# Optimization experiments

Hardware: AMD Instinct MI355X
Metric: run time of the kernel (lower is better)

## Reference

```python
import jax, jax.numpy as jnp
from jax import lax
import numpy as np

B, HW = 256, 64          # batch, image side (grayscale)
L, E, K = 32, 64, 8192   # latent_size, embedding_size, num_embeddings
DN = ('NHWC', 'HWIO', 'NHWC')


def setup_inputs() -> dict:
    key = jax.random.key(0)
    ks = jax.random.split(key, 21)
    n = lambda k, shape, s=0.05: (jax.random.normal(k, shape, jnp.float32) * s)
    return {
        'x': jax.random.uniform(ks[0], (B, HW, HW), jnp.float32),
        # encoder convs (SAME, stride 2): 64->32->16->8
        'enc_w1': n(ks[1], (4, 4, 1, 32)),   'enc_b1': jnp.zeros((32,), jnp.float32),
        'enc_w2': n(ks[2], (4, 4, 32, 64)),  'enc_b2': jnp.zeros((64,), jnp.float32),
        'enc_w3': n(ks[3], (4, 4, 64, 128)), 'enc_b3': jnp.zeros((128,), jnp.float32),
        # encoder dense: flatten 8*8*128=8192 -> 512 -> L*E=2048
        'fc_w': n(ks[4], (8192, 512), 0.02), 'fc_b': jnp.zeros((512,), jnp.float32),
        'ffc_w': n(ks[5], (512, L * E), 0.02), 'ffc_b': jnp.zeros((L * E,), jnp.float32),
        # VQ codebook
        'embeds': n(ks[6], (K, E), 0.02),
        # decoder dense: 2048 -> 512, then 1x1x512 feature map
        'dec_fc_w': n(ks[7], (L * E, 512), 0.02), 'dec_fc_b': jnp.zeros((512,), jnp.float32),
        # decoder conv_transpose VALID: 1->4->16->64
        'dec_w1': n(ks[8], (4, 4, 512, 256)),  'dec_b1': jnp.zeros((256,), jnp.float32),
        'dec_w2': n(ks[9], (4, 4, 256, 128)),  'dec_b2': jnp.zeros((128,), jnp.float32),
        'dec_w3': n(ks[10], (4, 4, 128, 1)),   'dec_b3': jnp.zeros((1,), jnp.float32),
    }


def _conv(h, w, b, s):
    return jax.nn.relu(lax.conv_general_dilated(h, w, (s, s), 'SAME', dimension_numbers=DN) + b)


def reference(x, enc_w1, enc_b1, enc_w2, enc_b2, enc_w3, enc_b3,
              fc_w, fc_b, ffc_w, ffc_b, embeds,
              dec_fc_w, dec_fc_b, dec_w1, dec_b1, dec_w2, dec_b2, dec_w3, dec_b3):
    # ---- encoder ----
    h = x[..., None]                                   # (B,64,64,1)
    h = _conv(h, enc_w1, enc_b1, 2)                    # (B,32,32,32)
    h = _conv(h, enc_w2, enc_b2, 2)                    # (B,16,16,64)
    h = _conv(h, enc_w3, enc_b3, 2)                    # (B,8,8,128)
    h = h.reshape(h.shape[0], -1)                      # (B,8192)
    h = jax.nn.relu(h @ fc_w + fc_b)                   # (B,512)
    pred = jax.nn.relu(h @ ffc_w + ffc_b).reshape(-1, L, E)  # (B,L,E)
    # ---- VQ middle: nearest codebook entry (argmin of L2 norm == argmin of squared dist) ----
    d2 = (jnp.sum(pred * pred, axis=-1, keepdims=True)
          - 2.0 * jnp.einsum('ble,ke->blk', pred, embeds)
          + jnp.sum(embeds * embeds, axis=-1))         # (B,L,K)
    classes = jnp.argmin(d2, axis=-1)                  # (B,L) int
    collected = embeds[classes]                        # (B,L,E) gather
    h = collected.reshape(-1, L * E)                   # (B,2048)
    # ---- decoder ----
    h = jax.nn.relu(h @ dec_fc_w + dec_fc_b)           # (B,512)
    h = h[:, None, None, :]                            # (B,1,1,512)
    h = jax.nn.relu(lax.conv_transpose(h, dec_w1, (1, 1), 'VALID', dimension_numbers=DN) + dec_b1)  # (B,4,4,256)
    h = jax.nn.relu(lax.conv_transpose(h, dec_w2, (4, 4), 'VALID', dimension_numbers=DN) + dec_b2)  # (B,16,16,128)
    out = lax.conv_transpose(h, dec_w3, (4, 4), 'VALID', dimension_numbers=DN) + dec_b3             # (B,64,64,1)
    return out  # L2 loss_type: output_t = logits_t
```

## Files before the change

kernel.cpp:

```cpp
#include <hip/hip_runtime.h>
#include <cfloat>


typedef short bf16x8 __attribute__((ext_vector_type(8)));
typedef float f32x4 __attribute__((ext_vector_type(4)));
#define MFMA16(a, b, c) __builtin_amdgcn_mfma_f32_16x16x32_bf16(a, b, c, 0, 0, 0)

__device__ inline unsigned short f2bf(float x) {
  unsigned u = __float_as_uint(x);
  u += 0x7fffu + ((u >> 16) & 1u);
  return (unsigned short)(u >> 16);
}
__device__ inline float bf2f(unsigned short h) {
  return __uint_as_float(((unsigned)h) << 16);
}
__device__ inline void split3v(float v, unsigned short& hb, unsigned short& mb,
                               unsigned short& lb) {
  hb = f2bf(v);
  float r1 = v - bf2f(hb);
  mb = f2bf(r1);
  lb = f2bf(r1 - bf2f(mb));
}

#define PB0 12672
#define PB1 (PB0 + 13056)
#define PB2 (PB1 + 128)
#define PB3 (PB2 + 512)
#define PB4 (PB3 + 2048)
#define PB5 (PB4 + 32)
#define PB6 (PB5 + 4096)
#define PB7 (PB6 + 2048)
__global__ __launch_bounds__(256) void k_prep_early(
    const float* __restrict__ enc_w2, const float* __restrict__ enc_w3,
    const float* __restrict__ embeds, const float* __restrict__ dec_fc_w,
    const float* __restrict__ dec_w2, unsigned short* __restrict__ h1base,
    unsigned short* __restrict__ h2base, unsigned short* __restrict__ Wp2H,
    unsigned short* __restrict__ Wp2M, unsigned short* __restrict__ Wp2L,
    unsigned short* __restrict__ Wp3H, unsigned short* __restrict__ Wp3M,
    unsigned short* __restrict__ Wp3L, unsigned short* __restrict__ eB,
    float* __restrict__ n2, unsigned short* __restrict__ Bp_dfc,
    unsigned short* __restrict__ Bp_d2) {
  int blk = blockIdx.x;
  int t = threadIdx.x;
  if (blk < PB0) {
    int li = blk * 256 + t;
    int bc = li & 8191;
    int rest = li >> 13;
    int i = rest % 132, plane = rest / 132;
    int b = bc >> 5, c = bc & 31;
    int row, col;
    if (i < 34) { row = 0; col = i; }
    else if (i < 68) { row = 33; col = i - 34; }
    else { int j = i - 68; row = 1 + (j >> 1); col = (j & 1) ? 33 : 0; }
    h1base[(size_t)plane * 9469952 + ((size_t)(b * 34 + row) * 34 + col) * 32 + c] = 0;
  } else if (blk < PB1) {
    int li = (blk - PB0) * 256 + t;
    int bc = li & 16383;
    int rest = li >> 14;
    int i = rest % 68, plane = rest / 68;
    int b = bc >> 6, c = bc & 63;
    int row, col;
    if (i < 18) { row = 0; col = i; }
    else if (i < 36) { row = 17; col = i - 18; }
    else { int j = i - 36; row = 1 + (j >> 1); col = (j & 1) ? 17 : 0; }
    h2base[(size_t)plane * 5308416 + ((size_t)(b * 18 + row) * 18 + col) * 64 + c] = 0;
  } else if (blk < PB2) {
    int idx = (blk - PB1) * 256 + t;
    int j = idx & 7, lane = (idx >> 3) & 63, nt = (idx >> 9) & 3, s = idx >> 11;
    int ci = ((lane >> 4) << 3) + j, co = (nt << 4) + (lane & 15);
    unsigned short hb, mb, lb;
    split3v(enc_w2[(s * 32 + ci) * 64 + co], hb, mb, lb);
    Wp2H[idx] = hb; Wp2M[idx] = mb; Wp2L[idx] = lb;
  } else if (blk < PB3) {
    int idx = (blk - PB2) * 256 + t;
    int j = idx & 7, lane = (idx >> 3) & 63, ks = (idx >> 9) & 1;
    int nt = (idx >> 10) & 3, ch = (idx >> 12) & 1, s = idx >> 13;
    int ci = ks * 32 + ((lane >> 4) << 3) + j;
    int co = ch * 64 + (nt << 4) + (lane & 15);
    unsigned short hb, mb, lb;
    split3v(enc_w3[(s * 64 + ci) * 128 + co], hb, mb, lb);
    Wp3H[idx] = hb; Wp3M[idx] = mb; Wp3L[idx] = lb;
  } else if (blk < PB4) {
    int idx = (blk - PB3) * 256 + t;
    int j = idx & 7, lane = (idx >> 3) & 63;
    int f = idx >> 9;
    int nt = f & 3, ks = (f >> 2) & 1, kt = f >> 3;
    int code = kt * 64 + nt * 16 + (lane & 15);
    int k = ks * 32 + ((lane >> 4) << 3) + j;
    unsigned short hb, mb, lb;
    split3v(embeds[(size_t)code * 64 + k], hb, mb, lb);
    size_t base = (size_t)f * 1536 + lane * 8 + j;
    eB[base] = hb; eB[base + 512] = mb; eB[base + 1024] = lb;
  } else if (blk < PB5) {
    int k = (blk - PB4) * 256 + t;
    const float4* p = (const float4*)(embeds + (size_t)k * 64);
    float s0 = 0, s1 = 0, s2 = 0, s3 = 0;
#pragma unroll
    for (int j = 0; j < 16; ++j) {
      float4 v = p[j];
      s0 = fmaf(v.x, v.x, s0); s1 = fmaf(v.y, v.y, s1);
      s2 = fmaf(v.z, v.z, s2); s3 = fmaf(v.w, v.w, s3);
    }
    n2[k] = (s0 + s1) + (s2 + s3);
  } else if (blk < PB6) {
    int idx = (blk - PB5) * 256 + t;
    int j = idx & 7, lane = (idx >> 3) & 63;
    int f = idx >> 9;
    int ntg = f & 31;
    int kt = f >> 5;
    int k = kt * 32 + ((lane >> 4) << 3) + j;
    int n = ntg * 16 + (lane & 15);
    unsigned short hb, mb, lb;
    split3v(dec_fc_w[(size_t)k * 512 + n], hb, mb, lb);
    Bp_dfc[idx] = hb; Bp_dfc[idx + 1048576] = mb;
  } else if (blk < PB7) {
    int idx = (blk - PB6) * 256 + t;
    int j = idx & 7, lane = (idx >> 3) & 63;
    int f = idx >> 9;
    int ntg = f & 127;
    int kt = f >> 7;
    int k = kt * 32 + ((lane >> 4) << 3) + j;
    int n = ntg * 16 + (lane & 15);
    int o = n & 127, ru = n >> 7;
    int r = ru >> 2, u = ru & 3;
    int sf = (3 - r) * 4 + (3 - u);
    unsigned short hb, mb, lb;
    split3v(dec_w2[(((size_t)sf * 256 + k) << 7) + o], hb, mb, lb);
    Bp_d2[idx] = hb; Bp_d2[idx + 524288] = mb;
  }
}

__global__ __launch_bounds__(256) void k_conv1(const float* __restrict__ x,
                                               const float* __restrict__ w,
                                               const float* __restrict__ bias,
                                               unsigned short* __restrict__ oH,
                                               unsigned short* __restrict__ oM,
                                               unsigned short* __restrict__ oL) {
  int b = blockIdx.x >> 5;
  int y = blockIdx.x & 31;
  int t = threadIdx.x;
  int c = t & 31;
  int xg = t >> 5;
  float acc[4] = {0.f, 0.f, 0.f, 0.f};
  for (int dy = 0; dy < 4; ++dy) {
    int iy = 2 * y + dy - 1;
    if (iy < 0 || iy >= 64) continue;
    const float* xrow = x + ((size_t)b * 64 + iy) * 64;
    for (int dx = 0; dx < 4; ++dx) {
      float wv = w[(dy * 4 + dx) * 32 + c];
#pragma unroll
      for (int i = 0; i < 4; ++i) {
        int ix = 8 * xg + 2 * i + dx - 1;
        float v = (ix >= 0 && ix < 64) ? xrow[ix] : 0.f;
        acc[i] = fmaf(v, wv, acc[i]);
      }
    }
  }
  float bv = bias[c];
#pragma unroll
  for (int i = 0; i < 4; ++i) {
    float v = acc[i] + bv;
    v = v > 0.f ? v : 0.f;
    unsigned short hb, mb, lb;
    split3v(v, hb, mb, lb);
    size_t o = ((size_t)(b * 34 + y + 1) * 34 + (4 * xg + i + 1)) * 32 + c;
    oH[o] = hb; oM[o] = mb; oL[o] = lb;
  }
}

__global__ __launch_bounds__(1024, 4) void k_conv2s(
    const unsigned short* __restrict__ aH, const unsigned short* __restrict__ aM,
    const unsigned short* __restrict__ aL, const unsigned short* __restrict__ wH,
    const unsigned short* __restrict__ wM, const unsigned short* __restrict__ wL,
    const float* __restrict__ bias, unsigned short* __restrict__ oH,
    unsigned short* __restrict__ oM, unsigned short* __restrict__ oL) {
  __shared__ unsigned short Bs[49152];
  int t = threadIdx.x;
  int wave = t >> 6, lane = t & 63;
  int l15 = lane & 15, quad = lane >> 4;
  int m0 = blockIdx.x * 256 + wave * 16;
  int p = m0 + l15;
  int b = p >> 8, y = (p >> 4) & 15, x = p & 15;
  f32x4 acc[4] = {};
#pragma unroll
  for (int hf = 0; hf < 2; ++hf) {
    if (hf) __syncthreads();
    {
      const unsigned short* s0 = wH + hf * 16384;
      const unsigned short* s1 = wM + hf * 16384;
      const unsigned short* s2 = wL + hf * 16384;
#pragma unroll
      for (int i = 0; i < 2; ++i) {
        int o8 = (i * 1024 + t) * 8;
        *(bf16x8*)(Bs + o8)         = *(const bf16x8*)(s0 + o8);
        *(bf16x8*)(Bs + 16384 + o8) = *(const bf16x8*)(s1 + o8);
        *(bf16x8*)(Bs + 32768 + o8) = *(const bf16x8*)(s2 + o8);
      }
    }
    __syncthreads();
#pragma unroll 4
    for (int sl = 0; sl < 8; ++sl) {
      int s = hf * 8 + sl;
      int dy = s >> 2, dx = s & 3;
      size_t aoff = ((size_t)(b * 34 + 2 * y + dy) * 34 + (2 * x + dx)) * 32 + quad * 8;
      bf16x8 ah = *(const bf16x8*)(aH + aoff);
      bf16x8 am = *(const bf16x8*)(aM + aoff);
      bf16x8 al = *(const bf16x8*)(aL + aoff);
#pragma unroll
      for (int nt = 0; nt < 4; ++nt) {
        const unsigned short* bp = Bs + ((sl * 4 + nt) * 64 + lane) * 8;
        bf16x8 bh = *(const bf16x8*)(bp);
        bf16x8 bm = *(const bf16x8*)(bp + 16384);
        bf16x8 bl = *(const bf16x8*)(bp + 32768);
        acc[nt] = MFMA16(am, bm, acc[nt]);
        acc[nt] = MFMA16(ah, bl, acc[nt]);
        acc[nt] = MFMA16(al, bh, acc[nt]);
        acc[nt] = MFMA16(ah, bm, acc[nt]);
        acc[nt] = MFMA16(am, bh, acc[nt]);
        acc[nt] = MFMA16(ah, bh, acc[nt]);
      }
    }
  }
#pragma unroll
  for (int r = 0; r < 4; ++r) {
    int pp = m0 + quad * 4 + r;
    int b2 = pp >> 8, yo = (pp >> 4) & 15, xo = pp & 15;
    size_t obase = ((size_t)(b2 * 18 + yo + 1) * 18 + (xo + 1)) * 64;
#pragma unroll
    for (int nt = 0; nt < 4; ++nt) {
      int co = nt * 16 + l15;
      float v = acc[nt][r] + bias[co];
      v = v > 0.f ? v : 0.f;
      unsigned short hb, mb, lb;
      split3v(v, hb, mb, lb);
      oH[obase + co] = hb; oM[obase + co] = mb; oL[obase + co] = lb;
    }
  }
}

__global__ __launch_bounds__(512, 2) void k_conv3s(
    const unsigned short* __restrict__ aH, const unsigned short* __restrict__ aM,
    const unsigned short* __restrict__ aL, const unsigned short* __restrict__ wH,
    const unsigned short* __restrict__ wM, const unsigned short* __restrict__ wL,
    float* __restrict__ part) {
  __shared__ unsigned short Bs[2][24576];
  int t = threadIdx.x;
  int wave = t >> 6, lane = t & 63;
  int l15 = lane & 15, quad = lane >> 4;
  int ch = wave & 1, mg = wave >> 1;
  int m0 = blockIdx.x * 128 + mg * 32;
  int z = blockIdx.y;
  f32x4 acc[2][4] = {};
  {
    const unsigned short* srcH = wH + (size_t)(z * 8) * 8192;
    const unsigned short* srcM = wM + (size_t)(z * 8) * 8192;
    const unsigned short* srcL = wL + (size_t)(z * 8) * 8192;
#pragma unroll
    for (int i = 0; i < 2; ++i) {
      int o8 = (i * 512 + t) * 8;
      *(bf16x8*)(&Bs[0][o8])         = *(const bf16x8*)(srcH + o8);
      *(bf16x8*)(&Bs[0][8192 + o8])  = *(const bf16x8*)(srcM + o8);
      *(bf16x8*)(&Bs[0][16384 + o8]) = *(const bf16x8*)(srcL + o8);
    }
  }
  __syncthreads();
#pragma unroll 2
  for (int si = 0; si < 8; ++si) {
    int s = z * 8 + si;
    int cur = si & 1, nxt = cur ^ 1;
    bf16x8 stg[6];
    if (si < 7) {
      const unsigned short* srcH = wH + (size_t)(s + 1) * 8192;
      const unsigned short* srcM = wM + (size_t)(s + 1) * 8192;
      const unsigned short* srcL = wL + (size_t)(s + 1) * 8192;
#pragma unroll
      for (int i = 0; i < 2; ++i) {
        int o8 = (i * 512 + t) * 8;
        stg[i]     = *(const bf16x8*)(srcH + o8);
        stg[2 + i] = *(const bf16x8*)(srcM + o8);
        stg[4 + i] = *(const bf16x8*)(srcL + o8);
      }
    }
    int dy = s >> 2, dx = s & 3;
    bf16x8 ah[2][2], am[2][2], al[2][2];
#pragma unroll
    for (int mt = 0; mt < 2; ++mt) {
      int p = m0 + mt * 16 + l15;
      int b = p >> 6, y = (p >> 3) & 7, x = p & 7;
      size_t base = ((size_t)(b * 18 + 2 * y + dy) * 18 + (2 * x + dx)) * 64 + quad * 8;
#pragma unroll
      for (int ks = 0; ks < 2; ++ks) {
        ah[mt][ks] = *(const bf16x8*)(aH + base + ks * 32);
        am[mt][ks] = *(const bf16x8*)(aM + base + ks * 32);
        al[mt][ks] = *(const bf16x8*)(aL + base + ks * 32);
      }
    }
#pragma unroll
    for (int nt = 0; nt < 4; ++nt)
#pragma unroll
      for (int ks = 0; ks < 2; ++ks) {
        const unsigned short* bp =
            &Bs[cur][((ch * 4 + nt) * 2 + ks) * 512 + lane * 8];
        bf16x8 bh = *(const bf16x8*)(bp);
        bf16x8 bm = *(const bf16x8*)(bp + 8192);
        bf16x8 bl = *(const bf16x8*)(bp + 16384);
#pragma unroll
        for (int mt = 0; mt < 2; ++mt) {
          acc[mt][nt] = MFMA16(am[mt][ks], bm, acc[mt][nt]);
          acc[mt][nt] = MFMA16(ah[mt][ks], bl, acc[mt][nt]);
          acc[mt][nt] = MFMA16(al[mt][ks], bh, acc[mt][nt]);
          acc[mt][nt] = MFMA16(ah[mt][ks], bm, acc[mt][nt]);
          acc[mt][nt] = MFMA16(am[mt][ks], bh, acc[mt][nt]);
          acc[mt][nt] = MFMA16(ah[mt][ks], bh, acc[mt][nt]);
        }
      }
    if (si < 7) {
#pragma unroll
      for (int i = 0; i < 2; ++i) {
        int o8 = (i * 512 + t) * 8;
        *(bf16x8*)(&Bs[nxt][o8])         = stg[i];
        *(bf16x8*)(&Bs[nxt][8192 + o8])  = stg[2 + i];
        *(bf16x8*)(&Bs[nxt][16384 + o8]) = stg[4 + i];
      }
    }
    __syncthreads();
  }
  float* Cp = part + (size_t)z * 2097152;
#pragma unroll
  for (int mt = 0; mt < 2; ++mt)
#pragma unroll
    for (int nt = 0; nt < 4; ++nt) {
      int co = ch * 64 + nt * 16 + l15;
#pragma unroll
      for (int r = 0; r < 4; ++r) {
        int pp = m0 + mt * 16 + quad * 4 + r;
        Cp[(size_t)pp * 128 + co] = acc[mt][nt][r];
      }
    }
}

#define FB0 8192
#define FB1 (FB0 + 16384)
__global__ __launch_bounds__(256) void k_prep_fc(
    const float* __restrict__ part, const float* __restrict__ enc_b3,
    unsigned short* __restrict__ h3H, unsigned short* __restrict__ h3M,
    unsigned short* __restrict__ h3L, const float* __restrict__ fc_w,
    unsigned short* __restrict__ Bp_fc) {
  int blk = blockIdx.x;
  int t = threadIdx.x;
  if (blk < FB0) {
    int idx = blk * 256 + t;
    float s = part[idx] + part[2097152 + idx] + enc_b3[idx & 127];
    s = s > 0.f ? s : 0.f;
    unsigned short hb, mb, lb;
    split3v(s, hb, mb, lb);
    h3H[idx] = hb; h3M[idx] = mb; h3L[idx] = lb;
  } else {
    int idx = (blk - FB0) * 256 + t;
    int j = idx & 7, lane = (idx >> 3) & 63;
    int f = idx >> 9;
    int ntg = f & 31;
    int kt = f >> 5;
    int k = kt * 32 + ((lane >> 4) << 3) + j;
    int n = ntg * 16 + (lane & 15);
    unsigned short hb, mb, lb;
    split3v(fc_w[(size_t)k * 512 + n], hb, mb, lb);
    Bp_fc[idx] = hb; Bp_fc[idx + 4194304] = mb; Bp_fc[idx + 8388608] = lb;
  }
}

#define WB0 4096
#define WB1 (WB0 + 8192)
__global__ __launch_bounds__(256) void k_prep_w2(
    const float* __restrict__ ffc_w, unsigned short* __restrict__ Bp_ffc,
    const float* __restrict__ dec_w1, unsigned short* __restrict__ Bp_d1) {
  int blk = blockIdx.x;
  int t = threadIdx.x;
  if (blk < WB0) {
    int idx = blk * 256 + t;
    int j = idx & 7, lane = (idx >> 3) & 63;
    int f = idx >> 9;
    int ntg = f & 127;
    int kt = f >> 7;
    int k = kt * 32 + ((lane >> 4) << 3) + j;
    int n = ntg * 16 + (lane & 15);
    unsigned short hb, mb, lb;
    split3v(ffc_w[(size_t)k * 2048 + n], hb, mb, lb);
    Bp_ffc[idx] = hb; Bp_ffc[idx + 1048576] = mb; Bp_ffc[idx + 2097152] = lb;
  } else {
    int idx = (blk - WB0) * 256 + t;
    int j = idx & 7, lane = (idx >> 3) & 63;
    int f = idx >> 9;
    int ntg = f & 255;
    int kt = f >> 8;
    int k = kt * 32 + ((lane >> 4) << 3) + j;
    int n = ntg * 16 + (lane & 15);
    int o = n & 255, ru = n >> 8;
    int r = ru >> 2, u = ru & 3;
    int sf = (3 - r) * 4 + (3 - u);
    unsigned short hb, mb, lb;
    split3v(dec_w1[(((size_t)sf * 512 + k) << 8) + o], hb, mb, lb);
    Bp_d1[idx] = hb; Bp_d1[idx + 2097152] = mb;
  }
}

template <int NP, int NTW>
__global__ __launch_bounds__(256) void k_mgemm(
    const unsigned short* __restrict__ A0, const unsigned short* __restrict__ A1,
    const unsigned short* __restrict__ A2, const unsigned short* __restrict__ Bp,
    float* __restrict__ C, const float* __restrict__ bias,
    int M, int N, int K, int bmask) {
  int S = gridDim.z;
  int Kc = K / S;
  int t = threadIdx.x;
  int wave = t >> 6, lane = t & 63;
  int l15 = lane & 15, quad = lane >> 4;
  int m0 = blockIdx.x * 64 + wave * 16;
  int n0 = blockIdx.y * (16 * NTW);
  int KT = K >> 5, NT = N >> 4;
  int kt0 = (blockIdx.z * Kc) >> 5;
  int ktn = Kc >> 5;
  size_t sstride = (size_t)KT * NT * 512;
  const unsigned short* arow0 = A0 + (size_t)(m0 + l15) * K + quad * 8;
  const unsigned short* arow1 = A1 + (size_t)(m0 + l15) * K + quad * 8;
  const unsigned short* arow2 = nullptr;
  if constexpr (NP == 3) arow2 = A2 + (size_t)(m0 + l15) * K + quad * 8;
  f32x4 acc[NTW] = {};
  for (int kt = kt0; kt < kt0 + ktn; ++kt) {
    bf16x8 ah = *(const bf16x8*)(arow0 + kt * 32);
    bf16x8 am = *(const bf16x8*)(arow1 + kt * 32);
    bf16x8 al;
    if constexpr (NP == 3) al = *(const bf16x8*)(arow2 + kt * 32);
    const unsigned short* bbase =
        Bp + ((size_t)kt * NT + (n0 >> 4)) * 512 + lane * 8;
#pragma unroll
    for (int nt = 0; nt < NTW; ++nt) {
      const unsigned short* bp = bbase + nt * 512;
      bf16x8 bh = *(const bf16x8*)(bp);
      bf16x8 bm = *(const bf16x8*)(bp + sstride);
      if constexpr (NP == 3) {
        bf16x8 bl = *(const bf16x8*)(bp + 2 * sstride);
        acc[nt] = MFMA16(am, bm, acc[nt]);
        acc[nt] = MFMA16(ah, bl, acc[nt]);
        acc[nt] = MFMA16(al, bh, acc[nt]);
        acc[nt] = MFMA16(ah, bm, acc[nt]);
        acc[nt] = MFMA16(am, bh, acc[nt]);
        acc[nt] = MFMA16(ah, bh, acc[nt]);
      } else {
        acc[nt] = MFMA16(ah, bm, acc[nt]);
        acc[nt] = MFMA16(am, bh, acc[nt]);
        acc[nt] = MFMA16(ah, bh, acc[nt]);
      }
    }
  }
  if (S == 1) {
#pragma unroll
    for (int nt = 0; nt < NTW; ++nt) {
      int n = n0 + nt * 16 + l15;
      float bv = bias[n & bmask];
#pragma unroll
      for (int r = 0; r < 4; ++r) {
        int m = m0 + quad * 4 + r;
        float v = acc[nt][r] + bv;
        C[(size_t)m * N + n] = v > 0.f ? v : 0.f;
      }
    }
  } else {
    float* Cp = C + (size_t)blockIdx.z * M * N;
#pragma unroll
    for (int nt = 0; nt < NTW; ++nt) {
      int n = n0 + nt * 16 + l15;
#pragma unroll
      for (int r = 0; r < 4; ++r) {
        int m = m0 + quad * 4 + r;
        Cp[(size_t)m * N + n] = acc[nt][r];
      }
    }
  }
}

template <int NPOUT>
__global__ __launch_bounds__(256) void k_sumrelu3(
    const float* __restrict__ part, const float* __restrict__ bias,
    unsigned short* __restrict__ oH, unsigned short* __restrict__ oM,
    unsigned short* __restrict__ oL, int MN, int bmask, int S) {
  int idx = blockIdx.x * 256 + threadIdx.x;
  float s = 0.f;
  for (int z = 0; z < S; ++z) s += part[(size_t)z * MN + idx];
  s += bias[idx & bmask];
  s = s > 0.f ? s : 0.f;
  unsigned short hb = f2bf(s);
  float r1 = s - bf2f(hb);
  unsigned short mb = f2bf(r1);
  oH[idx] = hb; oM[idx] = mb;
  if constexpr (NPOUT == 3) oL[idx] = f2bf(r1 - bf2f(mb));
}

__global__ __launch_bounds__(256) void k_vqmfma3(
    const unsigned short* __restrict__ pH, const unsigned short* __restrict__ pM,
    const unsigned short* __restrict__ pL, const unsigned short* __restrict__ eB,
    const float* __restrict__ n2, float* __restrict__ pbd, int* __restrict__ pbk) {
  int t = threadIdx.x;
  int wave = t >> 6, lane = t & 63;
  int l15 = lane & 15, quad = lane >> 4;
  int m0 = blockIdx.x * 128 + wave * 32;
  int z = blockIdx.y;
  bf16x8 ah[2][2], am[2][2], al[2][2];
#pragma unroll
  for (int mt = 0; mt < 2; ++mt) {
    size_t arow = (size_t)(m0 + mt * 16 + l15) * 64 + quad * 8;
#pragma unroll
    for (int ks = 0; ks < 2; ++ks) {
      ah[mt][ks] = *(const bf16x8*)(pH + arow + ks * 32);
      am[mt][ks] = *(const bf16x8*)(pM + arow + ks * 32);
      al[mt][ks] = *(const bf16x8*)(pL + arow + ks * 32);
    }
  }
  float bd[2][4]; int bk[2][4];
#pragma unroll
  for (int mt = 0; mt < 2; ++mt)
#pragma unroll
    for (int r = 0; r < 4; ++r) { bd[mt][r] = FLT_MAX; bk[mt][r] = 0; }
  for (int kt = z * 16; kt < z * 16 + 16; ++kt) {
    const unsigned short* bb = eB + (size_t)kt * 12288 + lane * 8;
    f32x4 acc[2][4] = {};
#pragma unroll
    for (int ks = 0; ks < 2; ++ks)
#pragma unroll
      for (int nt = 0; nt < 4; ++nt) {
        const unsigned short* bp = bb + ((ks * 4 + nt) * 3) * 512;
        bf16x8 bh = *(const bf16x8*)(bp);
        bf16x8 bm = *(const bf16x8*)(bp + 512);
        bf16x8 bl = *(const bf16x8*)(bp + 1024);
#pragma unroll
        for (int mt = 0; mt < 2; ++mt) {
          acc[mt][nt] = MFMA16(am[mt][ks], bm, acc[mt][nt]);
          acc[mt][nt] = MFMA16(ah[mt][ks], bl, acc[mt][nt]);
          acc[mt][nt] = MFMA16(al[mt][ks], bh, acc[mt][nt]);
          acc[mt][nt] = MFMA16(ah[mt][ks], bm, acc[mt][nt]);
          acc[mt][nt] = MFMA16(am[mt][ks], bh, acc[mt][nt]);
          acc[mt][nt] = MFMA16(ah[mt][ks], bh, acc[mt][nt]);
        }
      }
    int cb = kt * 64;
#pragma unroll
    for (int nt = 0; nt < 4; ++nt) {
      int code = cb + nt * 16 + l15;
      float nv = n2[code];
#pragma unroll
      for (int mt = 0; mt < 2; ++mt)
#pragma unroll
        for (int r = 0; r < 4; ++r) {
          float d = fmaf(-2.f, acc[mt][nt][r], nv);
          if (d < bd[mt][r]) { bd[mt][r] = d; bk[mt][r] = code; }
        }
    }
  }
#pragma unroll
  for (int mt = 0; mt < 2; ++mt)
#pragma unroll
    for (int r = 0; r < 4; ++r)
#pragma unroll
      for (int s = 1; s < 16; s <<= 1) {
        float od = __shfl_xor(bd[mt][r], s);
        int ok = __shfl_xor(bk[mt][r], s);
        if (od < bd[mt][r] || (od == bd[mt][r] && ok < bk[mt][r])) {
          bd[mt][r] = od; bk[mt][r] = ok;
        }
      }
  if (l15 == 0) {
#pragma unroll
    for (int mt = 0; mt < 2; ++mt)
#pragma unroll
      for (int r = 0; r < 4; ++r) {
        pbd[(size_t)z * 8192 + m0 + mt * 16 + quad * 4 + r] = bd[mt][r];
        pbk[(size_t)z * 8192 + m0 + mt * 16 + quad * 4 + r] = bk[mt][r];
      }
  }
}

__global__ __launch_bounds__(256) void k_vqgather(const float* __restrict__ pbd,
                                                  const int* __restrict__ pbk,
                                                  const float* __restrict__ embeds,
                                                  unsigned short* __restrict__ cH,
                                                  unsigned short* __restrict__ cM) {
  int idx = blockIdx.x * 256 + threadIdx.x;
  int m = idx >> 6;
  float bd = pbd[m]; int bk = pbk[m];
#pragma unroll
  for (int z = 1; z < 8; ++z) {
    float d = pbd[(size_t)z * 8192 + m]; int k = pbk[(size_t)z * 8192 + m];
    if (d < bd || (d == bd && k < bk)) { bd = d; bk = k; }
  }
  float v = embeds[(size_t)bk * 64 + (idx & 63)];
  unsigned short hb = f2bf(v);
  cH[idx] = hb;
  cM[idx] = f2bf(v - bf2f(hb));
}

__global__ __launch_bounds__(256) void k_dec3(const float* __restrict__ d2buf,
                                              const float* __restrict__ w3,
                                              const float* __restrict__ b3,
                                              float* __restrict__ out) {
  __shared__ float sx[16 * 129];
  __shared__ float wT[128 * 16];
  int b = blockIdx.x >> 4;
  int y = blockIdx.x & 15;
  int t = threadIdx.x;
#pragma unroll
  for (int j = 0; j < 8; ++j) {
    int idx = t + j * 256;
    int xx = idx >> 7, c = idx & 127;
    size_t m2 = ((size_t)b * 4 + (y >> 2)) * 4 + (xx >> 2);
    sx[xx * 129 + c] = d2buf[m2 * 2048 + ((y & 3) * 4 + (xx & 3)) * 128 + c];
  }
#pragma unroll
  for (int j = 0; j < 8; ++j) {
    int idx = t + j * 256;
    int c = idx >> 4, ru = idx & 15;
    int R = ru >> 2, U = ru & 3;
    wT[c * 16 + ru] = w3[((3 - R) * 4 + (3 - U)) * 128 + c];
  }
  __syncthreads();
  int xx = t >> 4, ru = t & 15;
  float a0 = 0, a1 = 0, a2 = 0, a3 = 0;
#pragma unroll 8
  for (int c = 0; c < 128; c += 4) {
    a0 = fmaf(sx[xx * 129 + c + 0], wT[(c + 0) * 16 + ru], a0);
    a1 = fmaf(sx[xx * 129 + c + 1], wT[(c + 1) * 16 + ru], a1);
    a2 = fmaf(sx[xx * 129 + c + 2], wT[(c + 2) * 16 + ru], a2);
    a3 = fmaf(sx[xx * 129 + c + 3], wT[(c + 3) * 16 + ru], a3);
  }
  float acc = (a0 + a1) + (a2 + a3) + b3[0];
  int R = ru >> 2, U = ru & 3;
  out[((size_t)b * 64 + 4 * y + R) * 64 + 4 * xx + U] = acc;
}

extern "C" void kernel_launch(void* const* d_in, const int* in_sizes, int n_in,
                              void* d_out, int out_size, void* d_ws, size_t ws_size,
                              hipStream_t stream) {
  const float* x        = (const float*)d_in[0];
  const float* enc_w1   = (const float*)d_in[1];
  const float* enc_b1   = (const float*)d_in[2];
  const float* enc_w2   = (const float*)d_in[3];
  const float* enc_b2   = (const float*)d_in[4];
  const float* enc_w3   = (const float*)d_in[5];
  const float* enc_b3   = (const float*)d_in[6];
  const float* fc_w     = (const float*)d_in[7];
  const float* fc_b     = (const float*)d_in[8];
  const float* ffc_w    = (const float*)d_in[9];
  const float* ffc_b    = (const float*)d_in[10];
  const float* embeds   = (const float*)d_in[11];
  const float* dec_fc_w = (const float*)d_in[12];
  const float* dec_fc_b = (const float*)d_in[13];
  const float* dec_w1   = (const float*)d_in[14];
  const float* dec_b1   = (const float*)d_in[15];
  const float* dec_w2   = (const float*)d_in[16];
  const float* dec_b2   = (const float*)d_in[17];
  const float* dec_w3   = (const float*)d_in[18];
  const float* dec_b3   = (const float*)d_in[19];
  float* outp = (float*)d_out;

  char* ws = (char*)d_ws;
  size_t off = 0;
  auto alloc = [&](size_t bytes) { size_t r = off; off = (off + bytes + 255) & ~(size_t)255; return r; };

  size_t RA = alloc(57147392);
  unsigned short* h1pH = (unsigned short*)(ws + RA);
  unsigned short* h1pM = (unsigned short*)(ws + RA + 18939904);
  unsigned short* h1pL = (unsigned short*)(ws + RA + 37879808);
  float* d2buf            = (float*)(ws + RA);
  float* partials         = (float*)(ws + RA + 33554432);
  unsigned short* Bp_d1   = (unsigned short*)(ws + RA + 41943040);
  unsigned short* d1H     = (unsigned short*)(ws + RA + 50331648);
  unsigned short* d1M     = (unsigned short*)(ws + RA + 52428800);
  unsigned short* hdH     = (unsigned short*)(ws + RA + 54525952);
  unsigned short* hdM     = (unsigned short*)(ws + RA + 54788096);
  unsigned short* cH      = (unsigned short*)(ws + RA + 55050240);
  unsigned short* cM      = (unsigned short*)(ws + RA + 56098816);

  size_t RB = alloc(31850496);
  unsigned short* h2pH = (unsigned short*)(ws + RB);
  unsigned short* h2pM = (unsigned short*)(ws + RB + 10616832);
  unsigned short* h2pL = (unsigned short*)(ws + RB + 21233664);
  unsigned short* Bp_fc = (unsigned short*)(ws + RB);
  unsigned short* pH    = (unsigned short*)(ws + RB + 28311552);
  unsigned short* pM    = (unsigned short*)(ws + RB + 29360128);
  unsigned short* pL    = (unsigned short*)(ws + RB + 30408704);

  size_t RC = alloc(12582912);
  unsigned short* h3H = (unsigned short*)(ws + RC);
  unsigned short* h3M = (unsigned short*)(ws + RC + 4194304);
  unsigned short* h3L = (unsigned short*)(ws + RC + 8388608);
  unsigned short* Bp_ffc = (unsigned short*)(ws + RC);
  unsigned short* hfcH   = (unsigned short*)(ws + RC + 6291456);
  unsigned short* hfcM   = (unsigned short*)(ws + RC + 6553600);
  unsigned short* hfcL   = (unsigned short*)(ws + RC + 6815744);

  unsigned short* eB     = (unsigned short*)(ws + alloc(3145728));
  unsigned short* Bp_dfc = (unsigned short*)(ws + alloc(4194304));
  unsigned short* Bp_d2  = (unsigned short*)(ws + alloc(2097152));
  float* n2buf   = (float*)(ws + alloc(32768));
  float* pbd     = (float*)(ws + alloc(262144));
  int*   pbk     = (int*)  (ws + alloc(262144));
  unsigned short* Wp2H = (unsigned short*)(ws + alloc(196608));
  unsigned short* Wp2M = Wp2H + 32768;
  unsigned short* Wp2L = Wp2M + 32768;
  unsigned short* Wp3H = (unsigned short*)(ws + alloc(786432));
  unsigned short* Wp3M = Wp3H + 131072;
  unsigned short* Wp3L = Wp3M + 131072;
  (void)ws_size; (void)in_sizes; (void)n_in; (void)out_size;

  k_prep_early<<<PB7, 256, 0, stream>>>(
      enc_w2, enc_w3, embeds, dec_fc_w, dec_w2, h1pH, h2pH,
      Wp2H, Wp2M, Wp2L, Wp3H, Wp3M, Wp3L, eB, n2buf, Bp_dfc, Bp_d2);

  k_conv1<<<8192, 256, 0, stream>>>(x, enc_w1, enc_b1, h1pH, h1pM, h1pL);
  k_conv2s<<<256, 1024, 0, stream>>>(h1pH, h1pM, h1pL, Wp2H, Wp2M, Wp2L,
                                     enc_b2, h2pH, h2pM, h2pL);
  k_conv3s<<<dim3(128, 2), 512, 0, stream>>>(h2pH, h2pM, h2pL,
                                             Wp3H, Wp3M, Wp3L, partials);
  k_prep_fc<<<FB1, 256, 0, stream>>>(partials, enc_b3, h3H, h3M, h3L,
                                     fc_w, Bp_fc);

  k_mgemm<3, 4><<<dim3(4, 8, 16), 256, 0, stream>>>(
      h3H, h3M, h3L, Bp_fc, partials, fc_b, 256, 512, 8192, 511);
  k_prep_w2<<<WB1, 256, 0, stream>>>(ffc_w, Bp_ffc, dec_w1, Bp_d1);
  k_sumrelu3<3><<<512, 256, 0, stream>>>(partials, fc_b, hfcH, hfcM, hfcL,
                                         131072, 511, 16);
  k_mgemm<3, 4><<<dim3(4, 32, 4), 256, 0, stream>>>(
      hfcH, hfcM, hfcL, Bp_ffc, partials, ffc_b, 256, 2048, 512, 2047);
  k_sumrelu3<3><<<2048, 256, 0, stream>>>(partials, ffc_b, pH, pM, pL,
                                          524288, 2047, 4);

  k_vqmfma3<<<dim3(64, 8), 256, 0, stream>>>(pH, pM, pL, eB, n2buf, pbd, pbk);
  k_vqgather<<<2048, 256, 0, stream>>>(pbd, pbk, embeds, cH, cM);

  k_mgemm<2, 4><<<dim3(4, 8, 16), 256, 0, stream>>>(
      cH, cM, nullptr, Bp_dfc, partials, dec_fc_b, 256, 512, 2048, 511);
  k_sumrelu3<2><<<512, 256, 0, stream>>>(partials, dec_fc_b, hdH, hdM, nullptr,
                                         131072, 511, 16);

  k_mgemm<2, 4><<<dim3(4, 64, 2), 256, 0, stream>>>(
      hdH, hdM, nullptr, Bp_d1, partials, dec_b1, 256, 4096, 512, 255);
  k_sumrelu3<2><<<4096, 256, 0, stream>>>(partials, dec_b1, d1H, d1M, nullptr,
                                          1048576, 255, 2);

  k_mgemm<2, 8><<<dim3(64, 16, 1), 256, 0, stream>>>(
      d1H, d1M, nullptr, Bp_d2, d2buf, dec_b2, 4096, 2048, 256, 127);

  k_dec3<<<4096, 256, 0, stream>>>(d2buf, dec_w3, dec_b3, outp);
}
```

Baseline: 431.8 us.

## Stage VQ codebook tiles through double-buffered LDS with register prefetch

The VQ distance kernel used to read codebook fragments straight from global memory in every wave. It now loads each 64-code tile cooperatively into a double-buffered shared-memory array, prefetching the next tile into registers while the MFMAs run on the current one. The launch bounds also request two blocks per SM. This cuts redundant global loads across the four waves and hides load latency, but it adds 48KB of LDS per block, a barrier every iteration, and extra register pressure that may limit occupancy.

```diff
diff --git a/kernel.cpp b/kernel.cpp
--- a/kernel.cpp
+++ b/kernel.cpp
@@ -496,10 +496,11 @@
   if constexpr (NPOUT == 3) oL[idx] = f2bf(r1 - bf2f(mb));
 }
 
-__global__ __launch_bounds__(256) void k_vqmfma3(
+__global__ __launch_bounds__(256, 2) void k_vqmfma3(
     const unsigned short* __restrict__ pH, const unsigned short* __restrict__ pM,
     const unsigned short* __restrict__ pL, const unsigned short* __restrict__ eB,
     const float* __restrict__ n2, float* __restrict__ pbd, int* __restrict__ pbk) {
+  __shared__ unsigned short Es[2][12288];
   int t = threadIdx.x;
   int wave = t >> 6, lane = t & 63;
   int l15 = lane & 15, quad = lane >> 4;
@@ -521,8 +522,28 @@
   for (int mt = 0; mt < 2; ++mt)
 #pragma unroll
     for (int r = 0; r < 4; ++r) { bd[mt][r] = FLT_MAX; bk[mt][r] = 0; }
-  for (int kt = z * 16; kt < z * 16 + 16; ++kt) {
-    const unsigned short* bb = eB + (size_t)kt * 12288 + lane * 8;
+  {
+    const unsigned short* src = eB + (size_t)(z * 16) * 12288;
+#pragma unroll
+    for (int i = 0; i < 6; ++i) {
+      int o8 = (i * 256 + t) * 8;
+      *(bf16x8*)(&Es[0][o8]) = *(const bf16x8*)(src + o8);
+    }
+  }
+  __syncthreads();
+  for (int ki = 0; ki < 16; ++ki) {
+    int kt = z * 16 + ki;
+    int cur = ki & 1, nxt = cur ^ 1;
+    bf16x8 stg[6];
+    if (ki < 15) {
+      const unsigned short* src = eB + (size_t)(kt + 1) * 12288;
+#pragma unroll
+      for (int i = 0; i < 6; ++i) {
+        int o8 = (i * 256 + t) * 8;
+        stg[i] = *(const bf16x8*)(src + o8);
+      }
+    }
+    const unsigned short* bb = &Es[cur][lane * 8];
     f32x4 acc[2][4] = {};
 #pragma unroll
     for (int ks = 0; ks < 2; ++ks)
@@ -555,6 +576,14 @@
           if (d < bd[mt][r]) { bd[mt][r] = d; bk[mt][r] = code; }
         }
     }
+    if (ki < 15) {
+#pragma unroll
+      for (int i = 0; i < 6; ++i) {
+        int o8 = (i * 256 + t) * 8;
+        *(bf16x8*)(&Es[nxt][o8]) = stg[i];
+      }
+    }
+    __syncthreads();
   }
 #pragma unroll
   for (int mt = 0; mt < 2; ++mt)
```

After: 425.7 us (median of 2 runs). Within noise of the previous version (-1.4%).
